# Kernel optimization log

Measured on AMD Instinct MI355X. Metric: run time of the kernel, lower is better.

Reference implementation:

```python
import jax, jax.numpy as jnp
import numpy as np


def setup_inputs() -> dict:
    key = jax.random.key(0)
    ks = jax.random.split(key, 7)
    B, C, T = 64, 2048, 256  # T must equal C // heads (see module's matmul(attn, v))
    s = 0.02
    return {
        "x": jax.random.normal(ks[0], (B, C, T), dtype=jnp.float32),
        "Wq": jax.random.normal(ks[1], (C, C), dtype=jnp.float32) * s,
        "bq": jax.random.normal(ks[2], (C,), dtype=jnp.float32) * s,
        "Wk": jax.random.normal(ks[3], (C, C), dtype=jnp.float32) * s,
        "bk": jax.random.normal(ks[4], (C,), dtype=jnp.float32) * s,
        "Wv": jax.random.normal(ks[5], (C, C), dtype=jnp.float32) * s,
        "bv": jax.random.normal(ks[6], (C,), dtype=jnp.float32) * s,
        "heads": 8,
    }


def reference(x, Wq, bq, Wk, bk, Wv, bv, heads):
    B, C, T = x.shape
    H = heads
    D = C // H  # must equal T for this module's math
    scale = float(D) ** -0.5

    def proj(W, b):
        # 1x1 Conv1d == per-timestep linear: out[b,o,t] = sum_c W[o,c] x[b,c,t] + b[o]
        return jnp.einsum('oc,bct->bot', W, x) + b[None, :, None]

    q = proj(Wq, bq).reshape(B, H, D, T).transpose(0, 1, 3, 2)  # (B,H,T,D)
    k = proj(Wk, bk).reshape(B, H, D, T).transpose(0, 1, 3, 2)  # (B,H,T,D)
    v = proj(Wv, bv).reshape(B, H, D, T)                         # (B,H,D,T), D==T

    attn = jax.nn.softmax(jnp.einsum('bhid,bhjd->bhij', q, k) * scale, axis=-1)  # (B,H,T,T)
    # Faithful to torch: matmul(attn, v) with v UNpermuted -> contract attn's last axis with v's D axis
    out = jnp.einsum('bhik,bhkj->bhij', attn, v)  # (B,H,T,T)
    return out.reshape(B, C, T)
```

## Files before the change

### kernel.cpp

```cpp
#include <hip/hip_runtime.h>


typedef __attribute__((ext_vector_type(8))) short    bf16x8;
typedef __attribute__((ext_vector_type(4))) float    f32x4;
typedef __attribute__((ext_vector_type(4))) unsigned short us4;
typedef __attribute__((ext_vector_type(8))) unsigned short us8;
typedef unsigned short u16;
typedef unsigned int   u32;

#define CC 2048
#define TT 256
#define BB 64
#define HH 8
#define DD 256

__device__ __forceinline__ u16 f2bf(float f) {
  u32 u = __builtin_bit_cast(u32, f);
  u32 r = (u + 0x7fffu + ((u >> 16) & 1u)) >> 16;
  return (u16)r;
}
__device__ __forceinline__ float bf2f(u16 b) {
  u32 u = ((u32)b) << 16;
  return __builtin_bit_cast(float, u);
}

__device__ __forceinline__ void async16(const void* g, void* l) {
  __builtin_amdgcn_global_load_lds(
      (const __attribute__((address_space(1))) u32*)g,
      (__attribute__((address_space(3))) u32*)l, 16, 0, 0);
}

__global__ __launch_bounds__(256) void wconv_kernel(
    const float* __restrict__ w0, const float* __restrict__ w1,
    const float* __restrict__ w2, u16* __restrict__ dst) {
  int p = blockIdx.y;
  const float* s = (p == 0) ? w0 : (p == 1) ? w1 : w2;
  size_t i = ((size_t)blockIdx.x * 256 + threadIdx.x) * 4;
  float4 v = *(const float4*)(s + i);
  us4 o = {f2bf(v.x), f2bf(v.y), f2bf(v.z), f2bf(v.w)};
  *(us4*)(dst + (size_t)p * CC * CC + i) = o;
}

__global__ __launch_bounds__(256) void xt_kernel(
    const float* __restrict__ x, u16* __restrict__ xT) {
  __shared__ float tile[64][68];
  int t0 = blockIdx.x * 64;
  int c0 = blockIdx.y * 64;
  int b  = blockIdx.z;
  int tid = threadIdx.x;
  int lr = tid >> 4;
  int lc = (tid & 15) * 4;
  const float* src = x + ((size_t)b * CC + c0) * TT + t0;
#pragma unroll
  for (int s = 0; s < 4; ++s) {
    int c = s * 16 + lr;
    float4 v = *(const float4*)(src + (size_t)c * TT + lc);
    *(float4*)&tile[c][lc] = v;
  }
  __syncthreads();
  int t  = tid >> 2;
  int cb = (tid & 3) * 16;
  u16 tmp[16];
#pragma unroll
  for (int e = 0; e < 16; ++e) tmp[e] = f2bf(tile[cb + e][t]);
  u16* dst = xT + ((size_t)b * TT + t0 + t) * CC + c0 + cb;
  *(us8*)dst       = *(const us8*)&tmp[0];
  *(us8*)(dst + 8) = *(const us8*)&tmp[8];
}

__global__ __launch_bounds__(256) void proj_kernel(
    const u16* __restrict__ Wbf, const u16* __restrict__ xT,
    const float* __restrict__ bq, const float* __restrict__ bk,
    const float* __restrict__ bv, u16* __restrict__ qkv) {
  __shared__ __align__(16) u16 As[128 * 32];
  __shared__ __align__(16) u16 Bs[128 * 32];
  int tid = threadIdx.x;
  int m0 = blockIdx.x * 128;
  int t0 = blockIdx.y * 128;
  int z  = blockIdx.z;
  int proj = z >> 6;
  int b    = z & 63;
  const u16* A = Wbf + (size_t)proj * CC * CC;
  const u16* X = xT + (size_t)b * TT * CC;
  const float* bias = (proj == 0) ? bq : (proj == 1) ? bk : bv;
  u16* outp = qkv + (size_t)proj * BB * CC * TT;

  int lane = tid & 63, w = tid >> 6;
  int wm = w >> 1, wn = w & 1;
  int ar = lane & 15, kq = lane >> 4;

  int arow = tid >> 2;
  int acol = (tid & 3) * 8;
  const u16* Abase = A + (size_t)(m0 + arow) * CC + acol;
  const u16* Xbase = X + (size_t)(t0 + arow) * CC + acol;

  f32x4 acc[4][4] = {};
  for (int k0 = 0; k0 < CC; k0 += 32) {
    async16(Abase + k0, As + tid * 8);
    async16(Abase + (size_t)64 * CC + k0, As + 2048 + tid * 8);
    async16(Xbase + k0, Bs + tid * 8);
    async16(Xbase + (size_t)64 * CC + k0, Bs + 2048 + tid * 8);
    __syncthreads();
    bf16x8 af[4], bfv[4];
#pragma unroll
    for (int mt = 0; mt < 4; ++mt)
      af[mt] = *(const bf16x8*)&As[(wm * 64 + mt * 16 + ar) * 32 + kq * 8];
#pragma unroll
    for (int nt = 0; nt < 4; ++nt)
      bfv[nt] = *(const bf16x8*)&Bs[(wn * 64 + nt * 16 + ar) * 32 + kq * 8];
#pragma unroll
    for (int mt = 0; mt < 4; ++mt)
#pragma unroll
      for (int nt = 0; nt < 4; ++nt)
        acc[mt][nt] = __builtin_amdgcn_mfma_f32_16x16x32_bf16(
            af[mt], bfv[nt], acc[mt][nt], 0, 0, 0);
    __syncthreads();
  }
#pragma unroll
  for (int mt = 0; mt < 4; ++mt) {
    int ob = m0 + wm * 64 + mt * 16 + kq * 4;
    float b0 = bias[ob], b1 = bias[ob + 1], b2 = bias[ob + 2], b3 = bias[ob + 3];
    int h = ob >> 8, d = ob & 255;
    u16* obase = outp + (((size_t)b * HH + h) * TT) * DD + d;
#pragma unroll
    for (int nt = 0; nt < 4; ++nt) {
      int t = t0 + wn * 64 + nt * 16 + ar;
      f32x4 v = acc[mt][nt];
      us4 pk = {f2bf(v[0] + b0), f2bf(v[1] + b1), f2bf(v[2] + b2),
                f2bf(v[3] + b3)};
      *(us4*)(obase + (size_t)t * DD) = pk;
    }
  }
}

__global__ __launch_bounds__(256) void attn_kernel(
    const u16* __restrict__ qkv, float* __restrict__ out) {
  __shared__ __align__(16) u16 As[64 * 32];
  __shared__ __align__(16) u16 Bs[256 * 32];
  __shared__ __align__(16) u16 Ps[64 * 264];
  __shared__ float rowpart[64][4];
  __shared__ float inv[64];

  int tid = threadIdx.x;
  int i0 = blockIdx.x * 64;
  int bh = blockIdx.y;
  const size_t hd = (size_t)TT * DD;
  const u16* Q = qkv + (size_t)bh * hd;
  const u16* K = qkv + (size_t)(BB * HH + bh) * hd;
  const u16* V = qkv + (size_t)(2 * BB * HH + bh) * hd;

  int lane = tid & 63, w = tid >> 6;
  int ar = lane & 15, kq = lane >> 4;
  int arow = tid >> 2, acol = (tid & 3) * 8;

  const u16* Qbase = Q + (size_t)(i0 + arow) * DD + acol;
  const u16* Kbase = K + (size_t)arow * DD + acol;
  const u16* Vbase = V + (size_t)arow * DD + acol;

  f32x4 acc[4][4] = {};
  for (int k0 = 0; k0 < DD; k0 += 32) {
    async16(Qbase + k0, As + tid * 8);
#pragma unroll
    for (int s = 0; s < 4; ++s)
      async16(Kbase + (size_t)(s * 64) * DD + k0, Bs + s * 2048 + tid * 8);
    __syncthreads();
    bf16x8 af[4], bfv[4];
#pragma unroll
    for (int mt = 0; mt < 4; ++mt)
      af[mt] = *(const bf16x8*)&As[(mt * 16 + ar) * 32 + kq * 8];
#pragma unroll
    for (int nt = 0; nt < 4; ++nt)
      bfv[nt] = *(const bf16x8*)&Bs[(w * 64 + nt * 16 + ar) * 32 + kq * 8];
#pragma unroll
    for (int mt = 0; mt < 4; ++mt)
#pragma unroll
      for (int nt = 0; nt < 4; ++nt)
        acc[mt][nt] = __builtin_amdgcn_mfma_f32_16x16x32_bf16(
            af[mt], bfv[nt], acc[mt][nt], 0, 0, 0);
    __syncthreads();
  }
  const float scale = 0.0625f;
#pragma unroll
  for (int mt = 0; mt < 4; ++mt) {
    float ps[4] = {0.f, 0.f, 0.f, 0.f};
#pragma unroll
    for (int nt = 0; nt < 4; ++nt) {
      f32x4 v = acc[mt][nt];
#pragma unroll
      for (int r = 0; r < 4; ++r) {
        float p = __expf(v[r] * scale);
        u16 pb = f2bf(p);
        Ps[(mt * 16 + kq * 4 + r) * 264 + (w * 64 + nt * 16 + ar)] = pb;
        ps[r] += bf2f(pb);
      }
    }
#pragma unroll
    for (int r = 0; r < 4; ++r) {
      float s = ps[r];
      s += __shfl_xor(s, 1, 64);
      s += __shfl_xor(s, 2, 64);
      s += __shfl_xor(s, 4, 64);
      s += __shfl_xor(s, 8, 64);
      if (ar == 0) rowpart[mt * 16 + kq * 4 + r][w] = s;
    }
  }
  __syncthreads();
  if (tid < 64) {
    float s = rowpart[tid][0] + rowpart[tid][1] + rowpart[tid][2] +
              rowpart[tid][3];
    inv[tid] = 1.0f / s;
  }
#pragma unroll
  for (int mt = 0; mt < 4; ++mt)
#pragma unroll
    for (int nt = 0; nt < 4; ++nt) acc[mt][nt] = (f32x4){0.f, 0.f, 0.f, 0.f};
  for (int k0 = 0; k0 < TT; k0 += 32) {
#pragma unroll
    for (int s = 0; s < 4; ++s)
      async16(Vbase + (size_t)(s * 64) * DD + k0, Bs + s * 2048 + tid * 8);
    __syncthreads();
    bf16x8 af[4], bfv[4];
#pragma unroll
    for (int mt = 0; mt < 4; ++mt)
      af[mt] = *(const bf16x8*)&Ps[(mt * 16 + ar) * 264 + k0 + kq * 8];
#pragma unroll
    for (int nt = 0; nt < 4; ++nt)
      bfv[nt] = *(const bf16x8*)&Bs[(w * 64 + nt * 16 + ar) * 32 + kq * 8];
#pragma unroll
    for (int mt = 0; mt < 4; ++mt)
#pragma unroll
      for (int nt = 0; nt < 4; ++nt)
        acc[mt][nt] = __builtin_amdgcn_mfma_f32_16x16x32_bf16(
            af[mt], bfv[nt], acc[mt][nt], 0, 0, 0);
    __syncthreads();
  }
  int b = bh >> 3, h = bh & 7;
  float* obase = out + ((size_t)b * CC + h * TT + i0) * TT;
#pragma unroll
  for (int mt = 0; mt < 4; ++mt)
#pragma unroll
    for (int r = 0; r < 4; ++r) {
      int m = mt * 16 + kq * 4 + r;
      float iv = inv[m];
#pragma unroll
      for (int nt = 0; nt < 4; ++nt) {
        int n = w * 64 + nt * 16 + ar;
        obase[(size_t)m * TT + n] = acc[mt][nt][r] * iv;
      }
    }
}

extern "C" void kernel_launch(void* const* d_in, const int* in_sizes, int n_in,
                              void* d_out, int out_size, void* d_ws,
                              size_t ws_size, hipStream_t stream) {
  const float* x  = (const float*)d_in[0];
  const float* Wq = (const float*)d_in[1];
  const float* bq = (const float*)d_in[2];
  const float* Wk = (const float*)d_in[3];
  const float* bk = (const float*)d_in[4];
  const float* Wv = (const float*)d_in[5];
  const float* bv = (const float*)d_in[6];
  float* out = (float*)d_out;

  char* ws = (char*)d_ws;
  u16* xT  = (u16*)ws;
  u16* Wbf = (u16*)(ws + 67108864);
  u16* qkv = (u16*)(ws + 67108864 + 25165824);

  wconv_kernel<<<dim3(4096, 3, 1), 256, 0, stream>>>(Wq, Wk, Wv, Wbf);
  xt_kernel<<<dim3(4, 32, 64), 256, 0, stream>>>(x, xT);
  proj_kernel<<<dim3(16, 2, 192), 256, 0, stream>>>(Wbf, xT, bq, bk, bv, qkv);
  attn_kernel<<<dim3(4, 512, 1), 256, 0, stream>>>(qkv, out);
}
```

Before: 866.9 us.

## Enlarge projection GEMM tile and use fragment-ordered shared memory layout

The projection kernel now computes a 128x256 output tile per block (the full T dimension) with a K-step of 64, so each loaded weight tile is reused across all timesteps and the grid shrinks. Shared memory staging is reordered so each 16-row by 8-column fragment is stored contiguously in MFMA lane order, which aims to remove LDS bank conflicts on fragment reads in both the projection and attention kernels. In exchange, accumulator registers double to 128 floats per thread and LDS use grows, which may limit occupancy despite the launch-bounds hint of two blocks.

```diff
diff --git a/kernel.cpp b/kernel.cpp
--- a/kernel.cpp
+++ b/kernel.cpp
@@ -68,16 +68,15 @@
   *(us8*)(dst + 8) = *(const us8*)&tmp[8];
 }
 
-__global__ __launch_bounds__(256) void proj_kernel(
+__global__ __launch_bounds__(256, 2) void proj_kernel(
     const u16* __restrict__ Wbf, const u16* __restrict__ xT,
     const float* __restrict__ bq, const float* __restrict__ bk,
     const float* __restrict__ bv, u16* __restrict__ qkv) {
-  __shared__ __align__(16) u16 As[128 * 32];
-  __shared__ __align__(16) u16 Bs[128 * 32];
+  __shared__ __align__(16) u16 As[128 * 64];
+  __shared__ __align__(16) u16 Bs[256 * 64];
   int tid = threadIdx.x;
   int m0 = blockIdx.x * 128;
-  int t0 = blockIdx.y * 128;
-  int z  = blockIdx.z;
+  int z  = blockIdx.y;
   int proj = z >> 6;
   int b    = z & 63;
   const u16* A = Wbf + (size_t)proj * CC * CC;
@@ -89,31 +88,36 @@
   int wm = w >> 1, wn = w & 1;
   int ar = lane & 15, kq = lane >> 4;
 
-  int arow = tid >> 2;
-  int acol = (tid & 3) * 8;
-  const u16* Abase = A + (size_t)(m0 + arow) * CC + acol;
-  const u16* Xbase = X + (size_t)(t0 + arow) * CC + acol;
-
-  f32x4 acc[4][4] = {};
-  for (int k0 = 0; k0 < CC; k0 += 32) {
-    async16(Abase + k0, As + tid * 8);
-    async16(Abase + (size_t)64 * CC + k0, As + 2048 + tid * 8);
-    async16(Xbase + k0, Bs + tid * 8);
-    async16(Xbase + (size_t)64 * CC + k0, Bs + 2048 + tid * 8);
-    __syncthreads();
-    bf16x8 af[4], bfv[4];
-#pragma unroll
-    for (int mt = 0; mt < 4; ++mt)
-      af[mt] = *(const bf16x8*)&As[(wm * 64 + mt * 16 + ar) * 32 + kq * 8];
-#pragma unroll
-    for (int nt = 0; nt < 4; ++nt)
-      bfv[nt] = *(const bf16x8*)&Bs[(wn * 64 + nt * 16 + ar) * 32 + kq * 8];
-#pragma unroll
-    for (int mt = 0; mt < 4; ++mt)
-#pragma unroll
-      for (int nt = 0; nt < 4; ++nt)
-        acc[mt][nt] = __builtin_amdgcn_mfma_f32_16x16x32_bf16(
-            af[mt], bfv[nt], acc[mt][nt], 0, 0, 0);
+  int srow  = ((tid >> 7) << 4) + (tid & 15);
+  int skcol = ((tid >> 4) & 7) * 8;
+  const u16* Abase = A + (size_t)(m0 + srow) * CC + skcol;
+  const u16* Xbase = X + (size_t)srow * CC + skcol;
+
+  f32x4 acc[4][8] = {};
+  for (int k0 = 0; k0 < CC; k0 += 64) {
+#pragma unroll
+    for (int c = 0; c < 4; ++c)
+      async16(Abase + (size_t)(c * 32) * CC + k0, As + c * 2048 + tid * 8);
+#pragma unroll
+    for (int c = 0; c < 8; ++c)
+      async16(Xbase + (size_t)(c * 32) * CC + k0, Bs + c * 2048 + tid * 8);
+    __syncthreads();
+#pragma unroll
+    for (int kk = 0; kk < 64; kk += 32) {
+      bf16x8 af[4], bfv[8];
+#pragma unroll
+      for (int mt = 0; mt < 4; ++mt)
+        af[mt] = *(const bf16x8*)&As[((wm * 4 + mt) * 128 + (kk >> 3) * 16 + lane) * 8];
+#pragma unroll
+      for (int nt = 0; nt < 8; ++nt)
+        bfv[nt] = *(const bf16x8*)&Bs[((wn * 8 + nt) * 128 + (kk >> 3) * 16 + lane) * 8];
+#pragma unroll
+      for (int mt = 0; mt < 4; ++mt)
+#pragma unroll
+        for (int nt = 0; nt < 8; ++nt)
+          acc[mt][nt] = __builtin_amdgcn_mfma_f32_16x16x32_bf16(
+              af[mt], bfv[nt], acc[mt][nt], 0, 0, 0);
+    }
     __syncthreads();
   }
 #pragma unroll
@@ -123,8 +127,8 @@
     int h = ob >> 8, d = ob & 255;
     u16* obase = outp + (((size_t)b * HH + h) * TT) * DD + d;
 #pragma unroll
-    for (int nt = 0; nt < 4; ++nt) {
-      int t = t0 + wn * 64 + nt * 16 + ar;
+    for (int nt = 0; nt < 8; ++nt) {
+      int t = wn * 128 + nt * 16 + ar;
       f32x4 v = acc[mt][nt];
       us4 pk = {f2bf(v[0] + b0), f2bf(v[1] + b1), f2bf(v[2] + b2),
                 f2bf(v[3] + b3)};
@@ -151,26 +155,27 @@
 
   int lane = tid & 63, w = tid >> 6;
   int ar = lane & 15, kq = lane >> 4;
-  int arow = tid >> 2, acol = (tid & 3) * 8;
-
-  const u16* Qbase = Q + (size_t)(i0 + arow) * DD + acol;
-  const u16* Kbase = K + (size_t)arow * DD + acol;
-  const u16* Vbase = V + (size_t)arow * DD + acol;
+
+  int srow  = ((tid >> 6) << 4) + (tid & 15);
+  int skcol = ((tid >> 4) & 3) * 8;
+  const u16* Qbase = Q + (size_t)(i0 + srow) * DD + skcol;
+  const u16* Kbase = K + (size_t)srow * DD + skcol;
+  const u16* Vbase = V + (size_t)srow * DD + skcol;
 
   f32x4 acc[4][4] = {};
   for (int k0 = 0; k0 < DD; k0 += 32) {
     async16(Qbase + k0, As + tid * 8);
 #pragma unroll
-    for (int s = 0; s < 4; ++s)
-      async16(Kbase + (size_t)(s * 64) * DD + k0, Bs + s * 2048 + tid * 8);
+    for (int c = 0; c < 4; ++c)
+      async16(Kbase + (size_t)(c * 64) * DD + k0, Bs + c * 2048 + tid * 8);
     __syncthreads();
     bf16x8 af[4], bfv[4];
 #pragma unroll
     for (int mt = 0; mt < 4; ++mt)
-      af[mt] = *(const bf16x8*)&As[(mt * 16 + ar) * 32 + kq * 8];
+      af[mt] = *(const bf16x8*)&As[(mt * 64 + lane) * 8];
 #pragma unroll
     for (int nt = 0; nt < 4; ++nt)
-      bfv[nt] = *(const bf16x8*)&Bs[(w * 64 + nt * 16 + ar) * 32 + kq * 8];
+      bfv[nt] = *(const bf16x8*)&Bs[((w * 4 + nt) * 64 + lane) * 8];
 #pragma unroll
     for (int mt = 0; mt < 4; ++mt)
 #pragma unroll
@@ -216,8 +221,8 @@
     for (int nt = 0; nt < 4; ++nt) acc[mt][nt] = (f32x4){0.f, 0.f, 0.f, 0.f};
   for (int k0 = 0; k0 < TT; k0 += 32) {
 #pragma unroll
-    for (int s = 0; s < 4; ++s)
-      async16(Vbase + (size_t)(s * 64) * DD + k0, Bs + s * 2048 + tid * 8);
+    for (int c = 0; c < 4; ++c)
+      async16(Vbase + (size_t)(c * 64) * DD + k0, Bs + c * 2048 + tid * 8);
     __syncthreads();
     bf16x8 af[4], bfv[4];
 #pragma unroll
@@ -225,7 +230,7 @@
       af[mt] = *(const bf16x8*)&Ps[(mt * 16 + ar) * 264 + k0 + kq * 8];
 #pragma unroll
     for (int nt = 0; nt < 4; ++nt)
-      bfv[nt] = *(const bf16x8*)&Bs[(w * 64 + nt * 16 + ar) * 32 + kq * 8];
+      bfv[nt] = *(const bf16x8*)&Bs[((w * 4 + nt) * 64 + lane) * 8];
 #pragma unroll
     for (int mt = 0; mt < 4; ++mt)
 #pragma unroll
@@ -269,6 +274,6 @@
 
   wconv_kernel<<<dim3(4096, 3, 1), 256, 0, stream>>>(Wq, Wk, Wv, Wbf);
   xt_kernel<<<dim3(4, 32, 64), 256, 0, stream>>>(x, xT);
-  proj_kernel<<<dim3(16, 2, 192), 256, 0, stream>>>(Wbf, xT, bq, bk, bv, qkv);
+  proj_kernel<<<dim3(16, 192), 256, 0, stream>>>(Wbf, xT, bq, bk, bv, qkv);
   attn_kernel<<<dim3(4, 512, 1), 256, 0, stream>>>(qkv, out);
 }
```

Result: slower. 967.9 us (+11.6%).
